# Kernel optimization log

Measured on AMD Instinct MI355X. Metric: run time of the kernel, lower is better.

Reference implementation:

```python
import jax, jax.numpy as jnp
import numpy as np

GRID_H, GRID_W = 20, 80   # character grid
GLYPH_H, GLYPH_W = 16, 8  # pixels per glyph
N_GLYPHS = 256


def setup_inputs() -> dict:
    key = jax.random.key(0)
    k1, k2 = jax.random.split(key)
    B = 128
    data = jax.random.uniform(k1, (B, GRID_H, GRID_W, 264), dtype=jnp.float32)
    char_matrix = jax.random.uniform(k2, (N_GLYPHS, GLYPH_H, GLYPH_W), dtype=jnp.float32)
    return {"data": data, "char_matrix": char_matrix}


def _handle_colors(color, bold):
    # bold in [B,20,80,1], color in [B,20,80,3]
    bold = 0.5 * bold + 0.5
    color = bold * color
    return color.reshape(-1, GRID_H, 1, GRID_W, 1, 3)


def reference(data, char_matrix):
    # split 264 channels: 256 one-hot glyph, fg_bold 1, fg_color 3, bg_bold 1, bg_color 3
    char_data = data[..., :256]
    fg_bold   = data[..., 256:257]
    fg_color  = data[..., 257:260]
    bg_bold   = data[..., 260:261]
    bg_color  = data[..., 261:264]

    fg = _handle_colors(fg_color, fg_bold)  # [B,20,1,80,1,3]
    bg = _handle_colors(bg_color, bg_bold)  # [B,20,1,80,1,3]

    # one-hot matmul lookup: [B,20,80,256] x [256,16,8] -> [B,20,80,16,8]
    raw = jnp.einsum('bhwc,cyx->bhwyx', char_data, char_matrix)
    # transpose to [B,20,16,80,8], add trailing channel dim
    raw = raw.transpose(0, 1, 3, 2, 4).reshape(-1, GRID_H, GLYPH_H, GRID_W, GLYPH_W, 1)

    pixel_map = raw * fg + (1.0 - raw) * bg  # [B,20,16,80,8,3]
    return pixel_map.reshape(-1, GRID_H * GLYPH_H, GRID_W * GLYPH_W, 3)  # [B,320,640,3]
```

## Files before the change

### kernel.cpp

```cpp
#include <hip/hip_runtime.h>

#define GRID_H 20
#define GRID_W 80
#define NCH 264
#define K 256
#define NPIX 128

typedef __attribute__((ext_vector_type(8))) short short8;
typedef __attribute__((ext_vector_type(4))) float f32x4;
typedef __attribute__((ext_vector_type(8))) unsigned short u16x8;

static __device__ __forceinline__ unsigned short f2bf(float f) {
    unsigned int u = __builtin_bit_cast(unsigned int, f);
    u += 0x7FFFu + ((u >> 16) & 1u);
    return (unsigned short)(u >> 16);
}

static __device__ __forceinline__ int bswz(int pl, int clbyte) {
    return (pl * 512 + clbyte) ^ ((pl & 7) << 4);
}

__global__ void prep_kernel(const float* __restrict__ cm,
                            unsigned short* __restrict__ ws) {
    int i = blockIdx.x * 256 + threadIdx.x;
    int p  = i & 127;
    int c8 = i >> 7;
    int hf = p >> 6, pl = p & 63;
    u16x8 pk;
    #pragma unroll
    for (int j = 0; j < 8; ++j) pk[j] = f2bf(cm[(c8 * 8 + j) * NPIX + p]);
    *reinterpret_cast<u16x8*>((char*)ws + hf * 32768 + bswz(pl, c8 * 16)) = pk;
}

template <bool USE_WS>
__global__ __launch_bounds__(320) void ansi_kernel(
        const float* __restrict__ data,
        const float* __restrict__ cm,
        const unsigned short* __restrict__ ws,
        float* __restrict__ out) {
    __shared__ alignas(16) unsigned char ldsB[32768];
    __shared__ alignas(16) float S[5][2][16][24];

    const int blk = blockIdx.x;
    const int b = blk / GRID_H;
    const int h = blk % GRID_H;
    const float* dbase = data + (size_t)(b * GRID_H + h) * GRID_W * NCH;
    const int t = threadIdx.x;
    const int wave = t >> 6;
    const int lane = t & 63;
    const int mrow = lane & 15;
    const int g    = lane >> 4;
    const int cell0 = wave * 16;

    float fb[6] = {0.f, 0.f, 0.f, 0.f, 0.f, 0.f};
    if (lane < 16) {
        const float* q = dbase + (size_t)(cell0 + lane) * NCH + 256;
        float4 a = *reinterpret_cast<const float4*>(q);
        float4 c = *reinterpret_cast<const float4*>(q + 4);
        float fs = 0.5f * a.x + 0.5f;
        float bs = 0.5f * c.x + 0.5f;
        fb[0] = bs * c.y; fb[1] = bs * c.z; fb[2] = bs * c.w;
        fb[3] = fs * a.y - fb[0];
        fb[4] = fs * a.z - fb[1];
        fb[5] = fs * a.w - fb[2];
    }
    float bgv[4][3], dv[4][3];
    #pragma unroll
    for (int r = 0; r < 4; ++r) {
        int srcl = g * 4 + r;
        #pragma unroll
        for (int j = 0; j < 3; ++j) {
            bgv[r][j] = __shfl(fb[j], srcl);
            dv[r][j]  = __shfl(fb[3 + j], srcl);
        }
    }

    const float* arow = dbase + (size_t)(cell0 + mrow) * NCH + g * 8;
    short8 apk[8];
    #pragma unroll
    for (int ks = 0; ks < 8; ++ks) {
        float4 a0 = *reinterpret_cast<const float4*>(arow + ks * 32);
        float4 a1 = *reinterpret_cast<const float4*>(arow + ks * 32 + 4);
        u16x8 ap;
        ap[0] = f2bf(a0.x); ap[1] = f2bf(a0.y); ap[2] = f2bf(a0.z); ap[3] = f2bf(a0.w);
        ap[4] = f2bf(a1.x); ap[5] = f2bf(a1.y); ap[6] = f2bf(a1.z); ap[7] = f2bf(a1.w);
        apk[ks] = __builtin_bit_cast(short8, ap);
    }

    f32x4 acc[8];
    #pragma unroll
    for (int n = 0; n < 8; ++n) acc[n] = (f32x4){0.f, 0.f, 0.f, 0.f};

    #pragma unroll
    for (int half = 0; half < 2; ++half) {
        if (USE_WS) {
            const char* src = (const char*)ws + half * 32768;
            #pragma unroll
            for (int it = 0; it < 6; ++it) {
                int j = it * 320 + t;
                __builtin_amdgcn_global_load_lds(
                    (const __attribute__((address_space(1))) void*)(src + (size_t)j * 16),
                    (__attribute__((address_space(3))) void*)&ldsB[(it * 320 + wave * 64) * 16],
                    16, 0, 0);
            }
            if (t < 128) {
                int j = 1920 + t;
                __builtin_amdgcn_global_load_lds(
                    (const __attribute__((address_space(1))) void*)(src + (size_t)j * 16),
                    (__attribute__((address_space(3))) void*)&ldsB[(1920 + wave * 64) * 16],
                    16, 0, 0);
            }
        } else {
            for (int i = t; i < 64 * 32; i += 320) {
                int pl = i & 63;
                int cg = i >> 6;
                const float* src = cm + (size_t)cg * 8 * NPIX + half * 64 + pl;
                u16x8 pk;
                #pragma unroll
                for (int j = 0; j < 8; ++j) pk[j] = f2bf(src[j * NPIX]);
                *reinterpret_cast<u16x8*>(&ldsB[bswz(pl, cg * 16)]) = pk;
            }
        }
        __syncthreads();

        #pragma unroll
        for (int ks = 0; ks < 8; ++ks) {
            const int kbase = ks * 32 + g * 8;
            #pragma unroll
            for (int n = 0; n < 4; ++n) {
                int pl = n * 16 + mrow;
                short8 bfrag = *reinterpret_cast<short8*>(&ldsB[bswz(pl, kbase * 2)]);
                acc[half * 4 + n] = __builtin_amdgcn_mfma_f32_16x16x32_bf16(
                    apk[ks], bfrag, acc[half * 4 + n], 0, 0, 0);
            }
        }
        if (half == 0) __syncthreads();
    }

    const int col = lane & 15;
    f32x4* out4 = (f32x4*)out;
    const size_t rowf4 = (size_t)(b * 320 + h * 16) * 480 + wave * 96;
    const int line_sel = col >> 3;
    const int x3 = (col & 7) * 3;

    #pragma unroll
    for (int pass = 0; pass < 8; ++pass) {
        #pragma unroll
        for (int r = 0; r < 4; ++r) {
            float raw = acc[pass][r];
            float* o = &S[wave][line_sel][r * 4 + g][x3];
            o[0] = bgv[r][0] + raw * dv[r][0];
            o[1] = bgv[r][1] + raw * dv[r][1];
            o[2] = bgv[r][2] + raw * dv[r][2];
        }
        const f32x4* Sw = (const f32x4*)&S[wave][0][0][0];
        #pragma unroll
        for (int q = 0; q < 3; ++q) {
            int j = q * 64 + lane;
            int line = (j >= 96) ? 1 : 0;
            int rem = j - 96 * line;
            int c = rem / 6;
            int s = rem - 6 * c;
            f32x4 v = Sw[line * 96 + ((c & 3) * 4 + (c >> 2)) * 6 + s];
            __builtin_nontemporal_store(
                v, &out4[rowf4 + (size_t)(pass * 2 + line) * 480 + rem]);
        }
    }
}

extern "C" void kernel_launch(void* const* d_in, const int* in_sizes, int n_in,
                              void* d_out, int out_size, void* d_ws, size_t ws_size,
                              hipStream_t stream) {
    (void)in_sizes; (void)n_in; (void)out_size;
    const float* data = (const float*)d_in[0];
    const float* cm   = (const float*)d_in[1];
    float* out        = (float*)d_out;
    const int nblocks = 128 * GRID_H;
    if (ws_size >= 65536) {
        prep_kernel<<<16, 256, 0, stream>>>(cm, (unsigned short*)d_ws);
        ansi_kernel<true><<<nblocks, 320, 0, stream>>>(
            data, cm, (const unsigned short*)d_ws, out);
    } else {
        ansi_kernel<false><<<nblocks, 320, 0, stream>>>(data, cm, nullptr, out);
    }
}
```

Before: 100.5 us.

## Process two glyph rows per block with double-buffered glyph matrix in LDS

```diff
diff --git a/kernel.cpp b/kernel.cpp
--- a/kernel.cpp
+++ b/kernel.cpp
@@ -38,13 +38,15 @@
         const float* __restrict__ cm,
         const unsigned short* __restrict__ ws,
         float* __restrict__ out) {
-    __shared__ alignas(16) unsigned char ldsB[32768];
+    __shared__ alignas(16) unsigned char ldsB[2][32768];
     __shared__ alignas(16) float S[5][2][16][24];
 
     const int blk = blockIdx.x;
-    const int b = blk / GRID_H;
-    const int h = blk % GRID_H;
-    const float* dbase = data + (size_t)(b * GRID_H + h) * GRID_W * NCH;
+    const int b  = blk / 10;
+    const int rp = blk % 10;
+    const int h0 = rp * 2;
+    const float* dbase0 = data + (size_t)(b * GRID_H + h0) * GRID_W * NCH;
+    const float* dbase1 = dbase0 + (size_t)GRID_W * NCH;
     const int t = threadIdx.x;
     const int wave = t >> 6;
     const int lane = t & 63;
@@ -52,118 +54,182 @@
     const int g    = lane >> 4;
     const int cell0 = wave * 16;
 
-    float fb[6] = {0.f, 0.f, 0.f, 0.f, 0.f, 0.f};
+    if (USE_WS) {
+        const char* src = (const char*)ws;
+        #pragma unroll
+        for (int it = 0; it < 6; ++it) {
+            int j = it * 320 + t;
+            __builtin_amdgcn_global_load_lds(
+                (const __attribute__((address_space(1))) void*)(src + (size_t)j * 16),
+                (__attribute__((address_space(3))) void*)&ldsB[0][(it * 320 + wave * 64) * 16],
+                16, 0, 0);
+        }
+        if (t < 128) {
+            int j = 1920 + t;
+            __builtin_amdgcn_global_load_lds(
+                (const __attribute__((address_space(1))) void*)(src + (size_t)j * 16),
+                (__attribute__((address_space(3))) void*)&ldsB[0][(1920 + wave * 64) * 16],
+                16, 0, 0);
+        }
+    } else {
+        for (int i = t; i < 64 * 32; i += 320) {
+            int pl = i & 63;
+            int cg = i >> 6;
+            const float* src = cm + (size_t)cg * 8 * NPIX + pl;
+            u16x8 pk;
+            #pragma unroll
+            for (int j = 0; j < 8; ++j) pk[j] = f2bf(src[j * NPIX]);
+            *reinterpret_cast<u16x8*>(&ldsB[0][bswz(pl, cg * 16)]) = pk;
+        }
+    }
+
+    float fb0[6] = {0.f,0.f,0.f,0.f,0.f,0.f}, fb1[6] = {0.f,0.f,0.f,0.f,0.f,0.f};
     if (lane < 16) {
-        const float* q = dbase + (size_t)(cell0 + lane) * NCH + 256;
-        float4 a = *reinterpret_cast<const float4*>(q);
-        float4 c = *reinterpret_cast<const float4*>(q + 4);
-        float fs = 0.5f * a.x + 0.5f;
-        float bs = 0.5f * c.x + 0.5f;
-        fb[0] = bs * c.y; fb[1] = bs * c.z; fb[2] = bs * c.w;
-        fb[3] = fs * a.y - fb[0];
-        fb[4] = fs * a.z - fb[1];
-        fb[5] = fs * a.w - fb[2];
-    }
-    float bgv[4][3], dv[4][3];
+        const float* q0 = dbase0 + (size_t)(cell0 + lane) * NCH + 256;
+        float4 a = *reinterpret_cast<const float4*>(q0);
+        float4 c = *reinterpret_cast<const float4*>(q0 + 4);
+        float fs = 0.5f * a.x + 0.5f, bs = 0.5f * c.x + 0.5f;
+        fb0[0] = bs * c.y; fb0[1] = bs * c.z; fb0[2] = bs * c.w;
+        fb0[3] = fs * a.y - fb0[0]; fb0[4] = fs * a.z - fb0[1]; fb0[5] = fs * a.w - fb0[2];
+        const float* q1 = q0 + (size_t)GRID_W * NCH;
+        float4 a1 = *reinterpret_cast<const float4*>(q1);
+        float4 c1 = *reinterpret_cast<const float4*>(q1 + 4);
+        float fs1 = 0.5f * a1.x + 0.5f, bs1 = 0.5f * c1.x + 0.5f;
+        fb1[0] = bs1 * c1.y; fb1[1] = bs1 * c1.z; fb1[2] = bs1 * c1.w;
+        fb1[3] = fs1 * a1.y - fb1[0]; fb1[4] = fs1 * a1.z - fb1[1]; fb1[5] = fs1 * a1.w - fb1[2];
+    }
+    float bgv0[4][3], dv0[4][3], bgv1[4][3], dv1[4][3];
     #pragma unroll
     for (int r = 0; r < 4; ++r) {
         int srcl = g * 4 + r;
         #pragma unroll
         for (int j = 0; j < 3; ++j) {
-            bgv[r][j] = __shfl(fb[j], srcl);
-            dv[r][j]  = __shfl(fb[3 + j], srcl);
-        }
-    }
-
-    const float* arow = dbase + (size_t)(cell0 + mrow) * NCH + g * 8;
-    short8 apk[8];
+            bgv0[r][j] = __shfl(fb0[j], srcl);
+            dv0[r][j]  = __shfl(fb0[3 + j], srcl);
+            bgv1[r][j] = __shfl(fb1[j], srcl);
+            dv1[r][j]  = __shfl(fb1[3 + j], srcl);
+        }
+    }
+
+    const float* arow0 = dbase0 + (size_t)(cell0 + mrow) * NCH + g * 8;
+    const float* arow1 = arow0 + (size_t)GRID_W * NCH;
+    short8 apk0[8], apk1[8];
     #pragma unroll
     for (int ks = 0; ks < 8; ++ks) {
-        float4 a0 = *reinterpret_cast<const float4*>(arow + ks * 32);
-        float4 a1 = *reinterpret_cast<const float4*>(arow + ks * 32 + 4);
+        float4 a0 = *reinterpret_cast<const float4*>(arow0 + ks * 32);
+        float4 a1 = *reinterpret_cast<const float4*>(arow0 + ks * 32 + 4);
         u16x8 ap;
-        ap[0] = f2bf(a0.x); ap[1] = f2bf(a0.y); ap[2] = f2bf(a0.z); ap[3] = f2bf(a0.w);
-        ap[4] = f2bf(a1.x); ap[5] = f2bf(a1.y); ap[6] = f2bf(a1.z); ap[7] = f2bf(a1.w);
-        apk[ks] = __builtin_bit_cast(short8, ap);
-    }
-
-    f32x4 acc[8];
-    #pragma unroll
-    for (int n = 0; n < 8; ++n) acc[n] = (f32x4){0.f, 0.f, 0.f, 0.f};
-
-    #pragma unroll
-    for (int half = 0; half < 2; ++half) {
-        if (USE_WS) {
-            const char* src = (const char*)ws + half * 32768;
-            #pragma unroll
-            for (int it = 0; it < 6; ++it) {
-                int j = it * 320 + t;
-                __builtin_amdgcn_global_load_lds(
-                    (const __attribute__((address_space(1))) void*)(src + (size_t)j * 16),
-                    (__attribute__((address_space(3))) void*)&ldsB[(it * 320 + wave * 64) * 16],
-                    16, 0, 0);
-            }
-            if (t < 128) {
-                int j = 1920 + t;
-                __builtin_amdgcn_global_load_lds(
-                    (const __attribute__((address_space(1))) void*)(src + (size_t)j * 16),
-                    (__attribute__((address_space(3))) void*)&ldsB[(1920 + wave * 64) * 16],
-                    16, 0, 0);
-            }
-        } else {
-            for (int i = t; i < 64 * 32; i += 320) {
-                int pl = i & 63;
-                int cg = i >> 6;
-                const float* src = cm + (size_t)cg * 8 * NPIX + half * 64 + pl;
-                u16x8 pk;
-                #pragma unroll
-                for (int j = 0; j < 8; ++j) pk[j] = f2bf(src[j * NPIX]);
-                *reinterpret_cast<u16x8*>(&ldsB[bswz(pl, cg * 16)]) = pk;
-            }
-        }
-        __syncthreads();
-
-        #pragma unroll
-        for (int ks = 0; ks < 8; ++ks) {
-            const int kbase = ks * 32 + g * 8;
-            #pragma unroll
-            for (int n = 0; n < 4; ++n) {
-                int pl = n * 16 + mrow;
-                short8 bfrag = *reinterpret_cast<short8*>(&ldsB[bswz(pl, kbase * 2)]);
-                acc[half * 4 + n] = __builtin_amdgcn_mfma_f32_16x16x32_bf16(
-                    apk[ks], bfrag, acc[half * 4 + n], 0, 0, 0);
-            }
-        }
-        if (half == 0) __syncthreads();
+        ap[0]=f2bf(a0.x); ap[1]=f2bf(a0.y); ap[2]=f2bf(a0.z); ap[3]=f2bf(a0.w);
+        ap[4]=f2bf(a1.x); ap[5]=f2bf(a1.y); ap[6]=f2bf(a1.z); ap[7]=f2bf(a1.w);
+        apk0[ks] = __builtin_bit_cast(short8, ap);
+        float4 b0 = *reinterpret_cast<const float4*>(arow1 + ks * 32);
+        float4 b1 = *reinterpret_cast<const float4*>(arow1 + ks * 32 + 4);
+        u16x8 bp;
+        bp[0]=f2bf(b0.x); bp[1]=f2bf(b0.y); bp[2]=f2bf(b0.z); bp[3]=f2bf(b0.w);
+        bp[4]=f2bf(b1.x); bp[5]=f2bf(b1.y); bp[6]=f2bf(b1.z); bp[7]=f2bf(b1.w);
+        apk1[ks] = __builtin_bit_cast(short8, bp);
+    }
+
+    f32x4 acc0[8], acc1[8];
+    #pragma unroll
+    for (int n = 0; n < 8; ++n) {
+        acc0[n] = (f32x4){0.f, 0.f, 0.f, 0.f};
+        acc1[n] = (f32x4){0.f, 0.f, 0.f, 0.f};
+    }
+
+    __syncthreads();
+
+    if (USE_WS) {
+        const char* src = (const char*)ws + 32768;
+        #pragma unroll
+        for (int it = 0; it < 6; ++it) {
+            int j = it * 320 + t;
+            __builtin_amdgcn_global_load_lds(
+                (const __attribute__((address_space(1))) void*)(src + (size_t)j * 16),
+                (__attribute__((address_space(3))) void*)&ldsB[1][(it * 320 + wave * 64) * 16],
+                16, 0, 0);
+        }
+        if (t < 128) {
+            int j = 1920 + t;
+            __builtin_amdgcn_global_load_lds(
+                (const __attribute__((address_space(1))) void*)(src + (size_t)j * 16),
+                (__attribute__((address_space(3))) void*)&ldsB[1][(1920 + wave * 64) * 16],
+                16, 0, 0);
+        }
+    } else {
+        for (int i = t; i < 64 * 32; i += 320) {
+            int pl = i & 63;
+            int cg = i >> 6;
+            const float* src = cm + (size_t)cg * 8 * NPIX + 64 + pl;
+            u16x8 pk;
+            #pragma unroll
+            for (int j = 0; j < 8; ++j) pk[j] = f2bf(src[j * NPIX]);
+            *reinterpret_cast<u16x8*>(&ldsB[1][bswz(pl, cg * 16)]) = pk;
+        }
+    }
+
+    #pragma unroll
+    for (int ks = 0; ks < 8; ++ks) {
+        const int kbase = ks * 32 + g * 8;
+        #pragma unroll
+        for (int n = 0; n < 4; ++n) {
+            int pl = n * 16 + mrow;
+            short8 bfrag = *reinterpret_cast<short8*>(&ldsB[0][bswz(pl, kbase * 2)]);
+            acc0[n] = __builtin_amdgcn_mfma_f32_16x16x32_bf16(apk0[ks], bfrag, acc0[n], 0, 0, 0);
+            acc1[n] = __builtin_amdgcn_mfma_f32_16x16x32_bf16(apk1[ks], bfrag, acc1[n], 0, 0, 0);
+        }
+    }
+
+    __syncthreads();
+
+    #pragma unroll
+    for (int ks = 0; ks < 8; ++ks) {
+        const int kbase = ks * 32 + g * 8;
+        #pragma unroll
+        for (int n = 0; n < 4; ++n) {
+            int pl = n * 16 + mrow;
+            short8 bfrag = *reinterpret_cast<short8*>(&ldsB[1][bswz(pl, kbase * 2)]);
+            acc0[4 + n] = __builtin_amdgcn_mfma_f32_16x16x32_bf16(apk0[ks], bfrag, acc0[4 + n], 0, 0, 0);
+            acc1[4 + n] = __builtin_amdgcn_mfma_f32_16x16x32_bf16(apk1[ks], bfrag, acc1[4 + n], 0, 0, 0);
+        }
     }
 
     const int col = lane & 15;
     f32x4* out4 = (f32x4*)out;
-    const size_t rowf4 = (size_t)(b * 320 + h * 16) * 480 + wave * 96;
     const int line_sel = col >> 3;
     const int x3 = (col & 7) * 3;
-
-    #pragma unroll
-    for (int pass = 0; pass < 8; ++pass) {
-        #pragma unroll
-        for (int r = 0; r < 4; ++r) {
-            float raw = acc[pass][r];
-            float* o = &S[wave][line_sel][r * 4 + g][x3];
-            o[0] = bgv[r][0] + raw * dv[r][0];
-            o[1] = bgv[r][1] + raw * dv[r][1];
-            o[2] = bgv[r][2] + raw * dv[r][2];
-        }
-        const f32x4* Sw = (const f32x4*)&S[wave][0][0][0];
-        #pragma unroll
-        for (int q = 0; q < 3; ++q) {
-            int j = q * 64 + lane;
-            int line = (j >= 96) ? 1 : 0;
-            int rem = j - 96 * line;
-            int c = rem / 6;
-            int s = rem - 6 * c;
-            f32x4 v = Sw[line * 96 + ((c & 3) * 4 + (c >> 2)) * 6 + s];
-            __builtin_nontemporal_store(
-                v, &out4[rowf4 + (size_t)(pass * 2 + line) * 480 + rem]);
+    const f32x4* Sw = (const f32x4*)&S[wave][0][0][0];
+
+    #pragma unroll
+    for (int row = 0; row < 2; ++row) {
+        const size_t rowf4 = (size_t)(b * 320 + (h0 + row) * 16) * 480 + wave * 96;
+        #pragma unroll
+        for (int pass = 0; pass < 8; ++pass) {
+            #pragma unroll
+            for (int r = 0; r < 4; ++r) {
+                float raw = row == 0 ? acc0[pass][r] : acc1[pass][r];
+                float bgr = row == 0 ? bgv0[r][0] : bgv1[r][0];
+                float bgg = row == 0 ? bgv0[r][1] : bgv1[r][1];
+                float bgb = row == 0 ? bgv0[r][2] : bgv1[r][2];
+                float d0  = row == 0 ? dv0[r][0]  : dv1[r][0];
+                float d1  = row == 0 ? dv0[r][1]  : dv1[r][1];
+                float d2  = row == 0 ? dv0[r][2]  : dv1[r][2];
+                float* o = &S[wave][line_sel][r * 4 + g][x3];
+                o[0] = bgr + raw * d0;
+                o[1] = bgg + raw * d1;
+                o[2] = bgb + raw * d2;
+            }
+            #pragma unroll
+            for (int q = 0; q < 3; ++q) {
+                int j = q * 64 + lane;
+                int line = (j >= 96) ? 1 : 0;
+                int rem = j - 96 * line;
+                int c = rem / 6;
+                int s = rem - 6 * c;
+                f32x4 v = Sw[line * 96 + ((c & 3) * 4 + (c >> 2)) * 6 + s];
+                __builtin_nontemporal_store(
+                    v, &out4[rowf4 + (size_t)(pass * 2 + line) * 480 + rem]);
+            }
         }
     }
 }
@@ -175,7 +241,7 @@
     const float* data = (const float*)d_in[0];
     const float* cm   = (const float*)d_in[1];
     float* out        = (float*)d_out;
-    const int nblocks = 128 * GRID_H;
+    const int nblocks = 128 * (GRID_H / 2);
     if (ws_size >= 65536) {
         prep_kernel<<<16, 256, 0, stream>>>(cm, (unsigned short*)d_ws);
         ansi_kernel<true><<<nblocks, 320, 0, stream>>>(
```

Result: slower. 103.2 us (+2.7%).

## Double-buffer glyph matrix in LDS and prefetch both halves early

Applied to the files above, without the earlier changes.

```diff
diff --git a/kernel.cpp b/kernel.cpp
--- a/kernel.cpp
+++ b/kernel.cpp
@@ -38,7 +38,7 @@
         const float* __restrict__ cm,
         const unsigned short* __restrict__ ws,
         float* __restrict__ out) {
-    __shared__ alignas(16) unsigned char ldsB[32768];
+    __shared__ alignas(16) unsigned char ldsB[2][32768];
     __shared__ alignas(16) float S[5][2][16][24];
 
     const int blk = blockIdx.x;
@@ -51,6 +51,35 @@
     const int mrow = lane & 15;
     const int g    = lane >> 4;
     const int cell0 = wave * 16;
+
+    if (USE_WS) {
+        const char* src = (const char*)ws;
+        #pragma unroll
+        for (int it = 0; it < 6; ++it) {
+            int j = it * 320 + t;
+            __builtin_amdgcn_global_load_lds(
+                (const __attribute__((address_space(1))) void*)(src + (size_t)j * 16),
+                (__attribute__((address_space(3))) void*)&ldsB[0][(it * 320 + wave * 64) * 16],
+                16, 0, 0);
+        }
+        if (t < 128) {
+            int j = 1920 + t;
+            __builtin_amdgcn_global_load_lds(
+                (const __attribute__((address_space(1))) void*)(src + (size_t)j * 16),
+                (__attribute__((address_space(3))) void*)&ldsB[0][(1920 + wave * 64) * 16],
+                16, 0, 0);
+        }
+    } else {
+        for (int i = t; i < 64 * 32; i += 320) {
+            int pl = i & 63;
+            int cg = i >> 6;
+            const float* src = cm + (size_t)cg * 8 * NPIX + pl;
+            u16x8 pk;
+            #pragma unroll
+            for (int j = 0; j < 8; ++j) pk[j] = f2bf(src[j * NPIX]);
+            *reinterpret_cast<u16x8*>(&ldsB[0][bswz(pl, cg * 16)]) = pk;
+        }
+    }
 
     float fb[6] = {0.f, 0.f, 0.f, 0.f, 0.f, 0.f};
     if (lane < 16) {
@@ -91,50 +120,61 @@
     #pragma unroll
     for (int n = 0; n < 8; ++n) acc[n] = (f32x4){0.f, 0.f, 0.f, 0.f};
 
-    #pragma unroll
-    for (int half = 0; half < 2; ++half) {
-        if (USE_WS) {
-            const char* src = (const char*)ws + half * 32768;
+    __syncthreads();
+
+    if (USE_WS) {
+        const char* src = (const char*)ws + 32768;
+        #pragma unroll
+        for (int it = 0; it < 6; ++it) {
+            int j = it * 320 + t;
+            __builtin_amdgcn_global_load_lds(
+                (const __attribute__((address_space(1))) void*)(src + (size_t)j * 16),
+                (__attribute__((address_space(3))) void*)&ldsB[1][(it * 320 + wave * 64) * 16],
+                16, 0, 0);
+        }
+        if (t < 128) {
+            int j = 1920 + t;
+            __builtin_amdgcn_global_load_lds(
+                (const __attribute__((address_space(1))) void*)(src + (size_t)j * 16),
+                (__attribute__((address_space(3))) void*)&ldsB[1][(1920 + wave * 64) * 16],
+                16, 0, 0);
+        }
+    } else {
+        for (int i = t; i < 64 * 32; i += 320) {
+            int pl = i & 63;
+            int cg = i >> 6;
+            const float* src = cm + (size_t)cg * 8 * NPIX + 64 + pl;
+            u16x8 pk;
             #pragma unroll
-            for (int it = 0; it < 6; ++it) {
-                int j = it * 320 + t;
-                __builtin_amdgcn_global_load_lds(
-                    (const __attribute__((address_space(1))) void*)(src + (size_t)j * 16),
-                    (__attribute__((address_space(3))) void*)&ldsB[(it * 320 + wave * 64) * 16],
-                    16, 0, 0);
-            }
-            if (t < 128) {
-                int j = 1920 + t;
-                __builtin_amdgcn_global_load_lds(
-                    (const __attribute__((address_space(1))) void*)(src + (size_t)j * 16),
-                    (__attribute__((address_space(3))) void*)&ldsB[(1920 + wave * 64) * 16],
-                    16, 0, 0);
-            }
-        } else {
-            for (int i = t; i < 64 * 32; i += 320) {
-                int pl = i & 63;
-                int cg = i >> 6;
-                const float* src = cm + (size_t)cg * 8 * NPIX + half * 64 + pl;
-                u16x8 pk;
-                #pragma unroll
-                for (int j = 0; j < 8; ++j) pk[j] = f2bf(src[j * NPIX]);
-                *reinterpret_cast<u16x8*>(&ldsB[bswz(pl, cg * 16)]) = pk;
-            }
-        }
-        __syncthreads();
-
-        #pragma unroll
-        for (int ks = 0; ks < 8; ++ks) {
-            const int kbase = ks * 32 + g * 8;
-            #pragma unroll
-            for (int n = 0; n < 4; ++n) {
-                int pl = n * 16 + mrow;
-                short8 bfrag = *reinterpret_cast<short8*>(&ldsB[bswz(pl, kbase * 2)]);
-                acc[half * 4 + n] = __builtin_amdgcn_mfma_f32_16x16x32_bf16(
-                    apk[ks], bfrag, acc[half * 4 + n], 0, 0, 0);
-            }
-        }
-        if (half == 0) __syncthreads();
+            for (int j = 0; j < 8; ++j) pk[j] = f2bf(src[j * NPIX]);
+            *reinterpret_cast<u16x8*>(&ldsB[1][bswz(pl, cg * 16)]) = pk;
+        }
+    }
+
+    #pragma unroll
+    for (int ks = 0; ks < 8; ++ks) {
+        const int kbase = ks * 32 + g * 8;
+        #pragma unroll
+        for (int n = 0; n < 4; ++n) {
+            int pl = n * 16 + mrow;
+            short8 bfrag = *reinterpret_cast<short8*>(&ldsB[0][bswz(pl, kbase * 2)]);
+            acc[n] = __builtin_amdgcn_mfma_f32_16x16x32_bf16(
+                apk[ks], bfrag, acc[n], 0, 0, 0);
+        }
+    }
+
+    __syncthreads();
+
+    #pragma unroll
+    for (int ks = 0; ks < 8; ++ks) {
+        const int kbase = ks * 32 + g * 8;
+        #pragma unroll
+        for (int n = 0; n < 4; ++n) {
+            int pl = n * 16 + mrow;
+            short8 bfrag = *reinterpret_cast<short8*>(&ldsB[1][bswz(pl, kbase * 2)]);
+            acc[4 + n] = __builtin_amdgcn_mfma_f32_16x16x32_bf16(
+                apk[ks], bfrag, acc[4 + n], 0, 0, 0);
+        }
     }
 
     const int col = lane & 15;
```

Result: no change. 101.7 us (+1.1%).
